# Optimization experiments

Measured on AMD Instinct MI355X. Metric: run time of the kernel, lower is better.

Reference implementation:

```python
import jax, jax.numpy as jnp
import numpy as np

EPS = 1e-5  # BatchNorm eps (eval mode, running stats mean=0, var=1)
BN_SCALE = 1.0 / np.sqrt(1.0 + EPS)


def setup_inputs() -> dict:
    key = jax.random.key(0)
    ks = jax.random.split(key, 5)
    N, T, C, V, K = 64, 300, 64, 25, 3
    x = jax.random.normal(ks[0], (N, T, C, V), dtype=jnp.float32)
    # G: Linear(T -> 2T, no bias), Linear(2T -> K, no bias)
    g_w1 = jax.random.normal(ks[1], (2 * T, T), dtype=jnp.float32) * (1.0 / np.sqrt(T))
    g_w2 = jax.random.normal(ks[2], (K, 2 * T), dtype=jnp.float32) * (1.0 / np.sqrt(2 * T))
    # L: Conv1d(C -> C//4, K, pad=K//2, no bias), Conv1d(C//4 -> C, 1, no bias)
    l_w1 = jax.random.normal(ks[3], (C // 4, C, K), dtype=jnp.float32) * (1.0 / np.sqrt(C * K))
    l_w2 = jax.random.normal(ks[4], (C, C // 4), dtype=jnp.float32) * (1.0 / np.sqrt(C // 4))
    return {"x": x, "g_w1": g_w1, "g_w2": g_w2, "l_w1": l_w1, "l_w2": l_w2}


def reference(x, g_w1, g_w2, l_w1, l_w2):
    # x: [N, T, C, V]; n_segment == T so n_batch == N
    N, T, C, V = x.shape
    K = g_w2.shape[0]
    pad = K // 2
    # new_x: [N, C, T, V]
    new_x = jnp.transpose(x, (0, 2, 1, 3))
    # adaptive avg pool over V -> [N, C, T]
    pooled = jnp.mean(new_x, axis=-1)

    # --- G branch: per-(n,c) temporal kernel of size K ---
    g_in = pooled.reshape(N * C, T)                         # [N*C, T]
    h = jnp.maximum(g_in @ g_w1.T * BN_SCALE, 0.0)          # Linear + BN(eval) + ReLU
    conv_kernel = jax.nn.softmax(h @ g_w2.T, axis=-1)       # [N*C, K]
    conv_kernel = conv_kernel.reshape(N, C, K)

    # --- L branch: local activation over time ---
    z = jax.lax.conv_general_dilated(
        pooled, l_w1, window_strides=(1,), padding=[(pad, pad)],
        dimension_numbers=("NCH", "OIH", "NCH"))              # [N, C//4, T]
    z = jnp.maximum(z * BN_SCALE, 0.0)
    local_act = jax.nn.sigmoid(jnp.einsum("nct,oc->not", z, l_w2))  # [N, C, T]

    new_x = new_x * local_act[..., None]                    # [N, C, T, V]

    # --- per-(n,c) depthwise temporal conv (groups = N*C) ---
    xpad = jnp.pad(new_x, ((0, 0), (0, 0), (pad, pad), (0, 0)))
    windows = jnp.stack([xpad[:, :, k:k + T, :] for k in range(K)], axis=-1)  # [N,C,T,V,K]
    out = jnp.einsum("nctvk,nck->nctv", windows, conv_kernel)

    return jnp.transpose(out, (0, 2, 1, 3))                 # [N, T, C, V]
```

## Files before the change

### kernel.cpp

```cpp
#include <hip/hip_runtime.h>
#include <hip/hip_bf16.h>
#include <math.h>

#define BN_SCALE_F 0.99999500003749969f

typedef short short8v __attribute__((ext_vector_type(8)));
typedef float float4v __attribute__((ext_vector_type(4)));


__global__ __launch_bounds__(320) void pool_kernel(const float* __restrict__ x,
                                                   const float* __restrict__ g_w1,
                                                   const float* __restrict__ l_w1,
                                                   float* __restrict__ pooledT,
                                                   __hip_bfloat16* __restrict__ w1b,
                                                   float* __restrict__ lw1r) {
  __shared__ float buf[6400];
  int bid = blockIdx.x;
  int tid = threadIdx.x;
  if (bid < 4800) {
    const float4* src = (const float4*)(x + (size_t)bid * 6400);
    float4* b4 = (float4*)buf;
#pragma unroll
    for (int it = 0; it < 5; ++it) {
      int i = tid + it * 320;
      b4[i] = src[i];
    }
    __syncthreads();
    int wave = tid >> 6;
    int c = tid & 63;
    if (wave < 4) {
      const float* p = buf + wave * 1600 + c * 25;
      float s = 0.f;
#pragma unroll
      for (int v = 0; v < 25; ++v) s += p[v];
      pooledT[(size_t)(bid * 4 + wave) * 64 + c] = s * 0.04f;
    }
  } else if (bid < 4816) {
    int b = bid - 4800;
    for (int i = b * 256 + tid; i < 608 * 320; i += 16 * 256) {
      int j = i / 320, k = i - j * 320;
      float v = (j < 600 && k < 300) ? g_w1[(size_t)j * 300 + k] : 0.f;
      w1b[i] = __float2bfloat16(v);
    }
  } else {
    for (int i = tid; i < 3072; i += 320) {
      int o = i / 192;
      int rem = i - o * 192;
      int c = rem / 3;
      int k = rem - c * 3;
      lw1r[c * 48 + o * 3 + k] = l_w1[i];
    }
  }
}

union GLSmem {
  struct {
    __hip_bfloat16 abuf[16][328];
    __hip_bfloat16 hbuf[16][612];
    float logits[48];
  } g;
  struct {
    float p[64][81];
    float z[75][20];
  } l;
};

__global__ __launch_bounds__(320) void gl_kernel(const float* __restrict__ pooledT,
                                                 const __hip_bfloat16* __restrict__ w1b,
                                                 const float* __restrict__ g_w2,
                                                 const float* __restrict__ lw1r,
                                                 const float* __restrict__ l_w2,
                                                 float* __restrict__ kern,
                                                 float* __restrict__ la) {
  __shared__ GLSmem sm;
  int bid = blockIdx.x;
  int tid = threadIdx.x;
  int wave = tid >> 6, lane = tid & 63;
  if (bid < 256) {
    int r0 = bid * 16;
    int n = bid >> 2;
    int c0 = (bid & 3) * 16;
    for (int i = tid; i < 5120; i += 320) {
      int tt = i >> 4;
      int cc = i & 15;
      float v = (tt < 300) ? pooledT[((size_t)n * 300 + tt) * 64 + c0 + cc] : 0.f;
      sm.g.abuf[cc][tt] = __float2bfloat16(v);
    }
    __syncthreads();

    int row16 = lane & 15;
    int k8 = (lane >> 4) * 8;

    float4v acc[8];
#pragma unroll
    for (int q = 0; q < 8; ++q) acc[q] = (float4v){0.f, 0.f, 0.f, 0.f};

    const short* pb = (const short*)w1b + k8;
    const short* pa = (const short*)&sm.g.abuf[row16][k8];

    for (int kt = 0; kt < 10; ++kt) {
      short8v av = *(const short8v*)(pa + kt * 32);
#pragma unroll
      for (int q = 0; q < 8; ++q) {
        int jt = wave + 5 * q;
        if (jt < 38) {
          short8v bv = *(const short8v*)(pb + (size_t)(jt * 16 + row16) * 320 + kt * 32);
          acc[q] = __builtin_amdgcn_mfma_f32_16x16x32_bf16(av, bv, acc[q], 0, 0, 0);
        }
      }
    }

#pragma unroll
    for (int q = 0; q < 8; ++q) {
      int jt = wave + 5 * q;
      if (jt < 38) {
        int col = jt * 16 + row16;
#pragma unroll
        for (int reg = 0; reg < 4; ++reg) {
          int i = (lane >> 4) * 4 + reg;
          sm.g.hbuf[i][col] = __float2bfloat16(fmaxf(acc[q][reg] * BN_SCALE_F, 0.f));
        }
      }
    }
    __syncthreads();

    for (int o = wave; o < 48; o += 5) {
      int r = o / 3, k = o - r * 3;
      float s = 0.f;
#pragma unroll
      for (int q = 0; q < 10; ++q) {
        int jj = lane + q * 64;
        if (jj < 600) s = fmaf(__bfloat162float(sm.g.hbuf[r][jj]), g_w2[k * 600 + jj], s);
      }
#pragma unroll
      for (int off = 1; off < 64; off <<= 1) s += __shfl_xor(s, off, 64);
      if (lane == 0) sm.g.logits[o] = s;
    }
    __syncthreads();
    if (tid < 16) {
      float a = sm.g.logits[tid * 3 + 0];
      float b = sm.g.logits[tid * 3 + 1];
      float c = sm.g.logits[tid * 3 + 2];
      float m = fmaxf(a, fmaxf(b, c));
      float ea = expf(a - m), eb = expf(b - m), ec = expf(c - m);
      float inv = 1.f / (ea + eb + ec);
      size_t o = (size_t)(r0 + tid) * 3;
      kern[o] = ea * inv;
      kern[o + 1] = eb * inv;
      kern[o + 2] = ec * inv;
    }
  } else {
    int bid2 = bid - 256;
    int n = bid2 >> 2;
    int tc = bid2 & 3;
    int t0 = tc * 75;
    for (int i = tid; i < 77 * 64; i += 320) {
      int tt = i >> 6, c = i & 63;
      int gt = t0 - 1 + tt;
      sm.l.p[c][tt] = (gt >= 0 && gt < 300) ? pooledT[((size_t)n * 300 + gt) * 64 + c] : 0.f;
    }
    __syncthreads();
    if (tid < 256) {
      int og = __builtin_amdgcn_readfirstlane(tid >> 6);
      int tl = tid & 63;
      float acc[4] = {0.f, 0.f, 0.f, 0.f};
      const float* wb = lw1r + og * 12;
      for (int c = 0; c < 64; ++c) {
        const float* wr = wb + c * 48;
        float pk0 = sm.l.p[c][tl];
        float pk1 = sm.l.p[c][tl + 1];
        float pk2 = sm.l.p[c][tl + 2];
#pragma unroll
        for (int oi = 0; oi < 4; ++oi) {
          acc[oi] = fmaf(wr[oi * 3 + 0], pk0, acc[oi]);
          acc[oi] = fmaf(wr[oi * 3 + 1], pk1, acc[oi]);
          acc[oi] = fmaf(wr[oi * 3 + 2], pk2, acc[oi]);
        }
      }
      float4 zv;
      zv.x = fmaxf(acc[0] * BN_SCALE_F, 0.f);
      zv.y = fmaxf(acc[1] * BN_SCALE_F, 0.f);
      zv.z = fmaxf(acc[2] * BN_SCALE_F, 0.f);
      zv.w = fmaxf(acc[3] * BN_SCALE_F, 0.f);
      *(float4*)(&sm.l.z[tl][og * 4]) = zv;
    } else {
      int lane5 = tid - 256;
      int og = lane5 >> 4;
      int tlo = lane5 & 15;
      if (tlo < 11) {
        int tl = 64 + tlo;
        float acc[4] = {0.f, 0.f, 0.f, 0.f};
        for (int c = 0; c < 64; ++c) {
          const float* wr = lw1r + c * 48 + og * 12;
          float pk0 = sm.l.p[c][tl];
          float pk1 = sm.l.p[c][tl + 1];
          float pk2 = sm.l.p[c][tl + 2];
#pragma unroll
          for (int oi = 0; oi < 4; ++oi) {
            acc[oi] = fmaf(wr[oi * 3 + 0], pk0, acc[oi]);
            acc[oi] = fmaf(wr[oi * 3 + 1], pk1, acc[oi]);
            acc[oi] = fmaf(wr[oi * 3 + 2], pk2, acc[oi]);
          }
        }
        float4 zv;
        zv.x = fmaxf(acc[0] * BN_SCALE_F, 0.f);
        zv.y = fmaxf(acc[1] * BN_SCALE_F, 0.f);
        zv.z = fmaxf(acc[2] * BN_SCALE_F, 0.f);
        zv.w = fmaxf(acc[3] * BN_SCALE_F, 0.f);
        *(float4*)(&sm.l.z[tl][og * 4]) = zv;
      }
    }
    __syncthreads();
    {
      int c = tid / 5;
      int ts = tid - c * 5;
      const float4* w2v = (const float4*)(l_w2 + c * 16);
      float4 wA = w2v[0], wB = w2v[1], wC = w2v[2], wD = w2v[3];
      float* outp = la + (size_t)(n * 64 + c) * 300 + t0;
      for (int it = 0; it < 15; ++it) {
        int tl = ts + it * 5;
        const float4* zv = (const float4*)(&sm.l.z[tl][0]);
        float4 zA = zv[0], zB = zv[1], zC = zv[2], zD = zv[3];
        float s = zA.x * wA.x + zA.y * wA.y + zA.z * wA.z + zA.w * wA.w;
        s += zB.x * wB.x + zB.y * wB.y + zB.z * wB.z + zB.w * wB.w;
        s += zC.x * wC.x + zC.y * wC.y + zC.z * wC.z + zC.w * wC.w;
        s += zD.x * wD.x + zD.y * wD.y + zD.z * wD.z + zD.w * wD.w;
        outp[tl] = 1.f / (1.f + expf(-s));
      }
    }
  }
}

__global__ __launch_bounds__(256) void tam_final_kernel(const float* __restrict__ x,
                                                        const float* __restrict__ la,
                                                        const float* __restrict__ kern,
                                                        float* __restrict__ out) {
  int bid = blockIdx.x;
  int n = bid >> 4;
  int rem = bid & 15;
  int tch = rem >> 1;
  int half = rem & 1;
  int cv4 = half * 256 + threadIdx.x;
  if (cv4 >= 400) return;
  int e0 = cv4 * 4;
  int c0 = e0 / 25;
  int c3 = (e0 + 3) / 25;
  bool s1 = ((e0 + 1) / 25) != c0;
  bool s2 = ((e0 + 2) / 25) != c0;
  bool s3 = (c3 != c0);
  const float* lap0 = la + (size_t)(n * 64 + c0) * 300;
  const float* lap1 = la + (size_t)(n * 64 + c3) * 300;
  const float* kp0 = kern + (size_t)(n * 64 + c0) * 3;
  const float* kp1 = kern + (size_t)(n * 64 + c3) * 3;
  float k00 = kp0[0], k01 = kp0[1], k02 = kp0[2];
  float k10 = kp1[0], k11 = kp1[1], k12 = kp1[2];
  float4 K0 = {k00, s1 ? k10 : k00, s2 ? k10 : k00, s3 ? k10 : k00};
  float4 K1 = {k01, s1 ? k11 : k01, s2 ? k11 : k01, s3 ? k11 : k01};
  float4 K2 = {k02, s1 ? k12 : k02, s2 ? k12 : k02, s3 ? k12 : k02};

  const float4* xp = (const float4*)(x + (size_t)n * 480000) + cv4;
  float4* op = (float4*)(out + (size_t)n * 480000) + cv4;

  int t0 = tch * 38;
  int tend = t0 + 38;
  if (tend > 300) tend = 300;

#define LAMUL(dst, t)                                        \
  {                                                          \
    float l0 = lap0[(t)];                                    \
    float l1 = lap1[(t)];                                    \
    float4 xv = xp[(size_t)(t) * 400];                       \
    dst.x = xv.x * l0;                                       \
    dst.y = xv.y * (s1 ? l1 : l0);                           \
    dst.z = xv.z * (s2 ? l1 : l0);                           \
    dst.w = xv.w * (s3 ? l1 : l0);                           \
  }

  float4 am, ac, an;
  if (t0 > 0) {
    LAMUL(am, t0 - 1);
  } else {
    am = {0.f, 0.f, 0.f, 0.f};
  }
  LAMUL(ac, t0);
  for (int t = t0; t < tend; ++t) {
    if (t + 1 < 300) {
      LAMUL(an, t + 1);
    } else {
      an = {0.f, 0.f, 0.f, 0.f};
    }
    float4 o;
    o.x = fmaf(am.x, K0.x, fmaf(ac.x, K1.x, an.x * K2.x));
    o.y = fmaf(am.y, K0.y, fmaf(ac.y, K1.y, an.y * K2.y));
    o.z = fmaf(am.z, K0.z, fmaf(ac.z, K1.z, an.z * K2.z));
    o.w = fmaf(am.w, K0.w, fmaf(ac.w, K1.w, an.w * K2.w));
    op[(size_t)t * 400] = o;
    am = ac;
    ac = an;
  }
#undef LAMUL
}

extern "C" void kernel_launch(void* const* d_in, const int* in_sizes, int n_in,
                              void* d_out, int out_size, void* d_ws, size_t ws_size,
                              hipStream_t stream) {
  const float* x = (const float*)d_in[0];
  const float* g_w1 = (const float*)d_in[1];
  const float* g_w2 = (const float*)d_in[2];
  const float* l_w1 = (const float*)d_in[3];
  const float* l_w2 = (const float*)d_in[4];
  float* out = (float*)d_out;
  float* ws = (float*)d_ws;
  float* pooledT = ws;
  float* kern = ws + 1228800;
  float* lact = ws + 1228800 + 12288;
  __hip_bfloat16* w1b = (__hip_bfloat16*)(ws + 2469888);
  float* lw1r = ws + 2469888 + 97280;

  hipLaunchKernelGGL(pool_kernel, dim3(4817), dim3(320), 0, stream, x, g_w1, l_w1,
                     pooledT, w1b, lw1r);
  hipLaunchKernelGGL(gl_kernel, dim3(512), dim3(320), 0, stream, pooledT, w1b,
                     g_w2, lw1r, l_w2, kern, lact);
  hipLaunchKernelGGL(tam_final_kernel, dim3(1024), dim3(256), 0, stream, x, lact, kern, out);
}
```

Baseline: 106.1 us.

## Fuse pool, G/L branch, and final conv into one cooperative kernel with grid syncs

```diff
diff --git a/kernel.cpp b/kernel.cpp
--- a/kernel.cpp
+++ b/kernel.cpp
@@ -1,59 +1,18 @@
 #include <hip/hip_runtime.h>
+#include <hip/hip_cooperative_groups.h>
 #include <hip/hip_bf16.h>
 #include <math.h>
 
+namespace cg = cooperative_groups;
+
 #define BN_SCALE_F 0.99999500003749969f
 
 typedef short short8v __attribute__((ext_vector_type(8)));
 typedef float float4v __attribute__((ext_vector_type(4)));
 
 
-__global__ __launch_bounds__(320) void pool_kernel(const float* __restrict__ x,
-                                                   const float* __restrict__ g_w1,
-                                                   const float* __restrict__ l_w1,
-                                                   float* __restrict__ pooledT,
-                                                   __hip_bfloat16* __restrict__ w1b,
-                                                   float* __restrict__ lw1r) {
-  __shared__ float buf[6400];
-  int bid = blockIdx.x;
-  int tid = threadIdx.x;
-  if (bid < 4800) {
-    const float4* src = (const float4*)(x + (size_t)bid * 6400);
-    float4* b4 = (float4*)buf;
-#pragma unroll
-    for (int it = 0; it < 5; ++it) {
-      int i = tid + it * 320;
-      b4[i] = src[i];
-    }
-    __syncthreads();
-    int wave = tid >> 6;
-    int c = tid & 63;
-    if (wave < 4) {
-      const float* p = buf + wave * 1600 + c * 25;
-      float s = 0.f;
-#pragma unroll
-      for (int v = 0; v < 25; ++v) s += p[v];
-      pooledT[(size_t)(bid * 4 + wave) * 64 + c] = s * 0.04f;
-    }
-  } else if (bid < 4816) {
-    int b = bid - 4800;
-    for (int i = b * 256 + tid; i < 608 * 320; i += 16 * 256) {
-      int j = i / 320, k = i - j * 320;
-      float v = (j < 600 && k < 300) ? g_w1[(size_t)j * 300 + k] : 0.f;
-      w1b[i] = __float2bfloat16(v);
-    }
-  } else {
-    for (int i = tid; i < 3072; i += 320) {
-      int o = i / 192;
-      int rem = i - o * 192;
-      int c = rem / 3;
-      int k = rem - c * 3;
-      lw1r[c * 48 + o * 3 + k] = l_w1[i];
-    }
-  }
-}
-
-union GLSmem {
+union MonoSmem {
+  float poolbuf[6400];
   struct {
     __hip_bfloat16 abuf[16][328];
     __hip_bfloat16 hbuf[16][612];
@@ -65,17 +24,61 @@
   } l;
 };
 
-__global__ __launch_bounds__(320) void gl_kernel(const float* __restrict__ pooledT,
-                                                 const __hip_bfloat16* __restrict__ w1b,
-                                                 const float* __restrict__ g_w2,
-                                                 const float* __restrict__ lw1r,
-                                                 const float* __restrict__ l_w2,
-                                                 float* __restrict__ kern,
-                                                 float* __restrict__ la) {
-  __shared__ GLSmem sm;
+__global__ __launch_bounds__(320) void mono_kernel(const float* __restrict__ x,
+                                                   const float* __restrict__ g_w1,
+                                                   const float* __restrict__ l_w1,
+                                                   const float* __restrict__ g_w2,
+                                                   const float* __restrict__ l_w2,
+                                                   float* __restrict__ pooledT,
+                                                   __hip_bfloat16* __restrict__ w1b,
+                                                   float* __restrict__ lw1r,
+                                                   float* __restrict__ kern,
+                                                   float* __restrict__ la,
+                                                   float* __restrict__ out) {
+  cg::grid_group grid = cg::this_grid();
+  __shared__ MonoSmem sm;
   int bid = blockIdx.x;
   int tid = threadIdx.x;
   int wave = tid >> 6, lane = tid & 63;
+
+  for (int u = bid; u < 4817; u += 512) {
+    if (u < 4800) {
+      const float4* src = (const float4*)(x + (size_t)u * 6400);
+      float4* b4 = (float4*)sm.poolbuf;
+#pragma unroll
+      for (int it = 0; it < 5; ++it) {
+        int i = tid + it * 320;
+        b4[i] = src[i];
+      }
+      __syncthreads();
+      if (wave < 4) {
+        const float* p = sm.poolbuf + wave * 1600 + lane * 25;
+        float s = 0.f;
+#pragma unroll
+        for (int v = 0; v < 25; ++v) s += p[v];
+        pooledT[(size_t)(u * 4 + wave) * 64 + lane] = s * 0.04f;
+      }
+    } else if (u < 4816) {
+      int b = u - 4800;
+      for (int i = b * 256 + tid; i < 608 * 320; i += 16 * 256) {
+        int j = i / 320, k = i - j * 320;
+        float v = (j < 600 && k < 300) ? g_w1[(size_t)j * 300 + k] : 0.f;
+        w1b[i] = __float2bfloat16(v);
+      }
+    } else {
+      for (int i = tid; i < 3072; i += 320) {
+        int o = i / 192;
+        int rem = i - o * 192;
+        int c = rem / 3;
+        int k = rem - c * 3;
+        lw1r[c * 48 + o * 3 + k] = l_w1[i];
+      }
+    }
+    __syncthreads();
+  }
+
+  grid.sync();
+
   if (bid < 256) {
     int r0 = bid * 16;
     int n = bid >> 2;
@@ -229,76 +232,75 @@
       }
     }
   }
-}
-
-__global__ __launch_bounds__(256) void tam_final_kernel(const float* __restrict__ x,
-                                                        const float* __restrict__ la,
-                                                        const float* __restrict__ kern,
-                                                        float* __restrict__ out) {
-  int bid = blockIdx.x;
-  int n = bid >> 4;
-  int rem = bid & 15;
-  int tch = rem >> 1;
-  int half = rem & 1;
-  int cv4 = half * 256 + threadIdx.x;
-  if (cv4 >= 400) return;
-  int e0 = cv4 * 4;
-  int c0 = e0 / 25;
-  int c3 = (e0 + 3) / 25;
-  bool s1 = ((e0 + 1) / 25) != c0;
-  bool s2 = ((e0 + 2) / 25) != c0;
-  bool s3 = (c3 != c0);
-  const float* lap0 = la + (size_t)(n * 64 + c0) * 300;
-  const float* lap1 = la + (size_t)(n * 64 + c3) * 300;
-  const float* kp0 = kern + (size_t)(n * 64 + c0) * 3;
-  const float* kp1 = kern + (size_t)(n * 64 + c3) * 3;
-  float k00 = kp0[0], k01 = kp0[1], k02 = kp0[2];
-  float k10 = kp1[0], k11 = kp1[1], k12 = kp1[2];
-  float4 K0 = {k00, s1 ? k10 : k00, s2 ? k10 : k00, s3 ? k10 : k00};
-  float4 K1 = {k01, s1 ? k11 : k01, s2 ? k11 : k01, s3 ? k11 : k01};
-  float4 K2 = {k02, s1 ? k12 : k02, s2 ? k12 : k02, s3 ? k12 : k02};
-
-  const float4* xp = (const float4*)(x + (size_t)n * 480000) + cv4;
-  float4* op = (float4*)(out + (size_t)n * 480000) + cv4;
-
-  int t0 = tch * 38;
-  int tend = t0 + 38;
-  if (tend > 300) tend = 300;
+
+  grid.sync();
+
+  {
+    int n = bid >> 3;
+    int tch = bid & 7;
+    int t0 = tch * 38;
+    int tend = t0 + 38;
+    if (tend > 300) tend = 300;
+
+#pragma unroll 1
+    for (int pass = 0; pass < 2; ++pass) {
+      int cv4 = tid + pass * 320;
+      if (cv4 >= 400) break;
+      int e0 = cv4 * 4;
+      int c0 = e0 / 25;
+      int c3 = (e0 + 3) / 25;
+      bool s1 = ((e0 + 1) / 25) != c0;
+      bool s2 = ((e0 + 2) / 25) != c0;
+      bool s3 = (c3 != c0);
+      const float* lap0 = la + (size_t)(n * 64 + c0) * 300;
+      const float* lap1 = la + (size_t)(n * 64 + c3) * 300;
+      const float* kp0 = kern + (size_t)(n * 64 + c0) * 3;
+      const float* kp1 = kern + (size_t)(n * 64 + c3) * 3;
+      float k00 = kp0[0], k01 = kp0[1], k02 = kp0[2];
+      float k10 = kp1[0], k11 = kp1[1], k12 = kp1[2];
+      float4 K0 = {k00, s1 ? k10 : k00, s2 ? k10 : k00, s3 ? k10 : k00};
+      float4 K1 = {k01, s1 ? k11 : k01, s2 ? k11 : k01, s3 ? k11 : k01};
+      float4 K2 = {k02, s1 ? k12 : k02, s2 ? k12 : k02, s3 ? k12 : k02};
+
+      const float4* xp = (const float4*)(x + (size_t)n * 480000) + cv4;
+      float4* op = (float4*)(out + (size_t)n * 480000) + cv4;
 
 #define LAMUL(dst, t)                                        \
-  {                                                          \
-    float l0 = lap0[(t)];                                    \
-    float l1 = lap1[(t)];                                    \
-    float4 xv = xp[(size_t)(t) * 400];                       \
-    dst.x = xv.x * l0;                                       \
-    dst.y = xv.y * (s1 ? l1 : l0);                           \
-    dst.z = xv.z * (s2 ? l1 : l0);                           \
-    dst.w = xv.w * (s3 ? l1 : l0);                           \
+      {                                                      \
+        float l0 = lap0[(t)];                                \
+        float l1 = lap1[(t)];                                \
+        float4 xv = xp[(size_t)(t) * 400];                   \
+        dst.x = xv.x * l0;                                   \
+        dst.y = xv.y * (s1 ? l1 : l0);                       \
+        dst.z = xv.z * (s2 ? l1 : l0);                       \
+        dst.w = xv.w * (s3 ? l1 : l0);                       \
+      }
+
+      float4 am, ac, an;
+      if (t0 > 0) {
+        LAMUL(am, t0 - 1);
+      } else {
+        am = {0.f, 0.f, 0.f, 0.f};
+      }
+      LAMUL(ac, t0);
+      for (int t = t0; t < tend; ++t) {
+        if (t + 1 < 300) {
+          LAMUL(an, t + 1);
+        } else {
+          an = {0.f, 0.f, 0.f, 0.f};
+        }
+        float4 o;
+        o.x = fmaf(am.x, K0.x, fmaf(ac.x, K1.x, an.x * K2.x));
+        o.y = fmaf(am.y, K0.y, fmaf(ac.y, K1.y, an.y * K2.y));
+        o.z = fmaf(am.z, K0.z, fmaf(ac.z, K1.z, an.z * K2.z));
+        o.w = fmaf(am.w, K0.w, fmaf(ac.w, K1.w, an.w * K2.w));
+        op[(size_t)t * 400] = o;
+        am = ac;
+        ac = an;
+      }
+#undef LAMUL
+    }
   }
-
-  float4 am, ac, an;
-  if (t0 > 0) {
-    LAMUL(am, t0 - 1);
-  } else {
-    am = {0.f, 0.f, 0.f, 0.f};
-  }
-  LAMUL(ac, t0);
-  for (int t = t0; t < tend; ++t) {
-    if (t + 1 < 300) {
-      LAMUL(an, t + 1);
-    } else {
-      an = {0.f, 0.f, 0.f, 0.f};
-    }
-    float4 o;
-    o.x = fmaf(am.x, K0.x, fmaf(ac.x, K1.x, an.x * K2.x));
-    o.y = fmaf(am.y, K0.y, fmaf(ac.y, K1.y, an.y * K2.y));
-    o.z = fmaf(am.z, K0.z, fmaf(ac.z, K1.z, an.z * K2.z));
-    o.w = fmaf(am.w, K0.w, fmaf(ac.w, K1.w, an.w * K2.w));
-    op[(size_t)t * 400] = o;
-    am = ac;
-    ac = an;
-  }
-#undef LAMUL
 }
 
 extern "C" void kernel_launch(void* const* d_in, const int* in_sizes, int n_in,
@@ -317,9 +319,9 @@
   __hip_bfloat16* w1b = (__hip_bfloat16*)(ws + 2469888);
   float* lw1r = ws + 2469888 + 97280;
 
-  hipLaunchKernelGGL(pool_kernel, dim3(4817), dim3(320), 0, stream, x, g_w1, l_w1,
-                     pooledT, w1b, lw1r);
-  hipLaunchKernelGGL(gl_kernel, dim3(512), dim3(320), 0, stream, pooledT, w1b,
-                     g_w2, lw1r, l_w2, kern, lact);
-  hipLaunchKernelGGL(tam_final_kernel, dim3(1024), dim3(256), 0, stream, x, lact, kern, out);
+  void* args[] = {(void*)&x, (void*)&g_w1, (void*)&l_w1, (void*)&g_w2, (void*)&l_w2,
+                  (void*)&pooledT, (void*)&w1b, (void*)&lw1r, (void*)&kern,
+                  (void*)&lact, (void*)&out};
+  hipLaunchCooperativeKernel((const void*)mono_kernel, dim3(512), dim3(320), args, 0,
+                             stream);
 }
```

New measurement: 240.8 us. 2.27x slower.
